# Performance work log

Measured on AMD Instinct MI355X. Metric: run time of the kernel, lower is better.

Reference implementation:

```python
import jax, jax.numpy as jnp
import numpy as np

EPS = 1e-8      # GumbelTopK background epsilon
TAU = 0.01      # relaxation temperature
NEG = -1e9      # mask-out value for already-selected patches
PATCH = (64, 64, 64)


def patchify(x, ps):
    """[B,C,H,W,D] -> [B*Hn*Wn*Dn, C, Hp, Wp, Dp] (non-overlapping tiles)."""
    B, C, H, W, D = x.shape
    hp, wp, dp = ps
    hn, wn, dn = H // hp, W // wp, D // dp
    x = x.reshape(B, C, hn, hp, wn, wp, dn, dp)
    x = x.transpose(0, 2, 4, 6, 1, 3, 5, 7)  # B,Hn,Wn,Dn,C,Hp,Wp,Dp
    return x.reshape(B * hn * wn * dn, C, hp, wp, dp)


def gumbel_topk(logit_flat, gumbel, k, tau):
    """Iterative Gumbel top-k: hard one-hots (stop-grad) + relaxed soft-hots."""
    perturbed = logit_flat + gumbel  # [B, N]

    def step(mask, _):
        s = jax.nn.softmax((perturbed + mask) / tau, axis=-1)  # [B, N]
        hard = jax.nn.one_hot(jnp.argmax(s, axis=-1), s.shape[-1], dtype=s.dtype)
        return mask + hard * NEG, (jax.lax.stop_gradient(hard), s)

    _, (one_hots, soft_hots) = jax.lax.scan(
        step, jnp.zeros_like(perturbed), None, length=k)
    return one_hots, soft_hots  # each [K, B, N]


def reference(image, label, logit, background_mask, gumbel, k):
    B = logit.shape[0]
    img_patches = patchify(image, PATCH)  # [N, C, 64,64,64]
    lab_patches = patchify(label, PATCH)  # [N, 1, 64,64,64]

    log_mask = jnp.log(jnp.maximum(1.0 - background_mask, EPS))
    masked_logit = logit + log_mask                       # [B,1,Hn,Wn,Dn]
    flat = masked_logit.reshape(B, -1)                    # [B, N]

    one_h, soft_h = gumbel_topk(flat, gumbel, k, TAU)     # [K,B,N]
    K = one_h.shape[0]
    one_f = one_h.reshape(K, -1)                          # [K, B*N]
    soft_f = soft_h.reshape(K, -1)

    # TRAIN mode: image weighted by one_hot*soft_hot, label (LAB) by one_hot only
    img_out = jnp.einsum('nchwd,kn->kchwd', img_patches, one_f * soft_f)
    lab_out = jnp.einsum('nchwd,kn->kchwd', lab_patches, one_f)
    return img_out, lab_out, masked_logit


def setup_inputs():
    key = jax.random.key(0)
    k1, k2, k3, k4, k5 = jax.random.split(key, 5)
    image = jax.random.normal(k1, (1, 4, 256, 256, 256), jnp.float32)
    label = jax.random.uniform(k2, (1, 1, 256, 256, 256), jnp.float32)
    logit = jax.random.normal(k3, (1, 1, 4, 4, 4), jnp.float32)
    background_mask = jax.random.uniform(k4, (1, 1, 4, 4, 4), jnp.float32)
    u = jax.random.uniform(k5, (1, 64), jnp.float32, 1e-6, 1.0 - 1e-6)
    gumbel = -jnp.log(-jnp.log(u))
    return {"image": image, "label": label, "logit": logit,
            "background_mask": background_mask, "gumbel": gumbel, "k": 8}
```

## Files before the change

### kernel.cpp

```cpp
#include <hip/hip_runtime.h>

#define TAU_INV 100.0f
#define EPSB    1e-8f
#define NEGV    -1e9f

typedef float v4f __attribute__((ext_vector_type(4)));

__global__ void stk_select(const float* __restrict__ logit,
                           const float* __restrict__ bg,
                           const float* __restrict__ gumbel,
                           float* __restrict__ ml_out,
                           int*   __restrict__ sel_idx,
                           float* __restrict__ sel_w,
                           int K) {
    int t = threadIdx.x;

    float lm = logf(fmaxf(1.0f - bg[t], EPSB));
    float ml = logit[t] + lm;
    ml_out[t] = ml;
    float pv = ml + gumbel[t];
    float mk = 0.0f;

    for (int k = 0; k < K; ++k) {
        float v   = pv + mk;
        float bv  = v;
        int   bi  = t;
        #pragma unroll
        for (int off = 32; off >= 1; off >>= 1) {
            float vo = __shfl_xor(bv, off);
            int   io = __shfl_xor(bi, off);
            if (vo > bv || (vo == bv && io < bi)) { bv = vo; bi = io; }
        }
        float e = __expf((v - bv) * TAU_INV);
        #pragma unroll
        for (int off = 32; off >= 1; off >>= 1)
            e += __shfl_xor(e, off);

        if (t == 0) {
            sel_idx[k] = bi;
            sel_w[k]   = 1.0f / e;
        }
        if (t == bi) mk += NEGV;
    }
}

__global__ void stk_gather(const v4f* __restrict__ img,
                           const v4f* __restrict__ lab,
                           v4f* __restrict__ out,
                           const int*   __restrict__ sel_idx,
                           const float* __restrict__ sel_w,
                           int nImg4, int nTot4) {
    int tid = blockIdx.x * blockDim.x + threadIdx.x;
    if (tid >= nTot4) return;

    if (tid < nImg4) {
        int v   = tid;
        int dp4 = v & 15;
        int wp  = (v >> 4)  & 63;
        int hp  = (v >> 10) & 63;
        int c   = (v >> 16) & 3;
        int k   = v >> 18;
        int n   = sel_idx[k];
        int hn  = n >> 4, wn = (n >> 2) & 3, dn = n & 3;
        int src = c * 4194304 + (hn * 64 + hp) * 16384 + (wn * 64 + wp) * 64 + dn * 16 + dp4;
        v4f d = __builtin_nontemporal_load(&img[src]);
        float w = sel_w[k];
        d *= w;
        __builtin_nontemporal_store(d, &out[tid]);
    } else {
        int u   = tid - nImg4;
        int dp4 = u & 15;
        int wp  = (u >> 4)  & 63;
        int hp  = (u >> 10) & 63;
        int k   = u >> 16;
        int n   = sel_idx[k];
        int hn  = n >> 4, wn = (n >> 2) & 3, dn = n & 3;
        int src = (hn * 64 + hp) * 16384 + (wn * 64 + wp) * 64 + dn * 16 + dp4;
        v4f d = __builtin_nontemporal_load(&lab[src]);
        __builtin_nontemporal_store(d, &out[tid]);
    }
}

extern "C" void kernel_launch(void* const* d_in, const int* in_sizes, int n_in,
                              void* d_out, int out_size, void* d_ws, size_t ws_size,
                              hipStream_t stream) {
    const float* image  = (const float*)d_in[0];
    const float* label  = (const float*)d_in[1];
    const float* logit  = (const float*)d_in[2];
    const float* bg     = (const float*)d_in[3];
    const float* gumbel = (const float*)d_in[4];
    int K = (out_size - 64) / (5 * 64 * 64 * 64);

    float* out     = (float*)d_out;
    int*   sel_idx = (int*)d_ws;
    float* sel_w   = (float*)((char*)d_ws + 64);
    float* ml_out  = out + (size_t)K * 1310720;

    stk_select<<<1, 64, 0, stream>>>(logit, bg, gumbel, ml_out, sel_idx, sel_w, K);

    int nImg4 = K * 4 * 65536;
    int nTot4 = nImg4 + K * 65536;
    int blocks = (nTot4 + 255) / 256;
    stk_gather<<<blocks, 256, 0, stream>>>((const v4f*)image, (const v4f*)label,
                                           (v4f*)out, sel_idx, sel_w, nImg4, nTot4);
}
```

Measured before the change: 352.4 us.

## Fuse top-k selection into gather kernel with per-block redundant selection

Merges the single-block selection kernel and the gather kernel into one launch. Every block recomputes the Gumbel top-k selection in its first wavefront and keeps the indices and weights in shared memory, so the second kernel launch and the global workspace round-trip go away. The gather becomes a grid-stride loop with four elements per thread, which cuts the block count by four. The cost is redundant selection work in every block, a serial K-step shuffle chain paid before each block's loads can start, and fewer blocks in flight.

```diff
diff --git a/kernel.cpp b/kernel.cpp
--- a/kernel.cpp
+++ b/kernel.cpp
@@ -6,78 +6,75 @@
 
 typedef float v4f __attribute__((ext_vector_type(4)));
 
-__global__ void stk_select(const float* __restrict__ logit,
-                           const float* __restrict__ bg,
-                           const float* __restrict__ gumbel,
-                           float* __restrict__ ml_out,
-                           int*   __restrict__ sel_idx,
-                           float* __restrict__ sel_w,
-                           int K) {
-    int t = threadIdx.x;
+__global__ __launch_bounds__(256) void stk_fused(
+    const float* __restrict__ logit,
+    const float* __restrict__ bg,
+    const float* __restrict__ gumbel,
+    const v4f*   __restrict__ img,
+    const v4f*   __restrict__ lab,
+    v4f*         __restrict__ out,
+    float*       __restrict__ ml_out,
+    int K, int nImg4, int nTot4)
+{
+    __shared__ int   s_idx[32];
+    __shared__ float s_w[32];
+    const int t = threadIdx.x;
 
-    float lm = logf(fmaxf(1.0f - bg[t], EPSB));
-    float ml = logit[t] + lm;
-    ml_out[t] = ml;
-    float pv = ml + gumbel[t];
-    float mk = 0.0f;
+    if (t < 64) {
+        float lm = logf(fmaxf(1.0f - bg[t], EPSB));
+        float ml = logit[t] + lm;
+        if (blockIdx.x == 0) ml_out[t] = ml;
+        float pv = ml + gumbel[t];
+        float mk = 0.0f;
 
-    for (int k = 0; k < K; ++k) {
-        float v   = pv + mk;
-        float bv  = v;
-        int   bi  = t;
-        #pragma unroll
-        for (int off = 32; off >= 1; off >>= 1) {
-            float vo = __shfl_xor(bv, off);
-            int   io = __shfl_xor(bi, off);
-            if (vo > bv || (vo == bv && io < bi)) { bv = vo; bi = io; }
+        for (int k = 0; k < K; ++k) {
+            float v  = pv + mk;
+            float bv = v;
+            int   bi = t;
+            #pragma unroll
+            for (int off = 32; off >= 1; off >>= 1) {
+                float vo = __shfl_xor(bv, off);
+                int   io = __shfl_xor(bi, off);
+                if (vo > bv || (vo == bv && io < bi)) { bv = vo; bi = io; }
+            }
+            float e = __expf((v - bv) * TAU_INV);
+            #pragma unroll
+            for (int off = 32; off >= 1; off >>= 1)
+                e += __shfl_xor(e, off);
+
+            if (t == 0) { s_idx[k] = bi; s_w[k] = 1.0f / e; }
+            if (t == bi) mk += NEGV;
         }
-        float e = __expf((v - bv) * TAU_INV);
-        #pragma unroll
-        for (int off = 32; off >= 1; off >>= 1)
-            e += __shfl_xor(e, off);
+    }
+    __syncthreads();
 
-        if (t == 0) {
-            sel_idx[k] = bi;
-            sel_w[k]   = 1.0f / e;
+    const int stride = gridDim.x * blockDim.x;
+    for (int tid = blockIdx.x * blockDim.x + t; tid < nTot4; tid += stride) {
+        if (tid < nImg4) {
+            int v   = tid;
+            int dp4 = v & 15;
+            int wp  = (v >> 4)  & 63;
+            int hp  = (v >> 10) & 63;
+            int c   = (v >> 16) & 3;
+            int k   = v >> 18;
+            int n   = s_idx[k];
+            int hn  = n >> 4, wn = (n >> 2) & 3, dn = n & 3;
+            int src = c * 4194304 + (hn * 64 + hp) * 16384 + (wn * 64 + wp) * 64 + dn * 16 + dp4;
+            v4f d = __builtin_nontemporal_load(&img[src]);
+            d *= s_w[k];
+            __builtin_nontemporal_store(d, &out[tid]);
+        } else {
+            int u   = tid - nImg4;
+            int dp4 = u & 15;
+            int wp  = (u >> 4)  & 63;
+            int hp  = (u >> 10) & 63;
+            int k   = u >> 16;
+            int n   = s_idx[k];
+            int hn  = n >> 4, wn = (n >> 2) & 3, dn = n & 3;
+            int src = (hn * 64 + hp) * 16384 + (wn * 64 + wp) * 64 + dn * 16 + dp4;
+            v4f d = __builtin_nontemporal_load(&lab[src]);
+            __builtin_nontemporal_store(d, &out[tid]);
         }
-        if (t == bi) mk += NEGV;
-    }
-}
-
-__global__ void stk_gather(const v4f* __restrict__ img,
-                           const v4f* __restrict__ lab,
-                           v4f* __restrict__ out,
-                           const int*   __restrict__ sel_idx,
-                           const float* __restrict__ sel_w,
-                           int nImg4, int nTot4) {
-    int tid = blockIdx.x * blockDim.x + threadIdx.x;
-    if (tid >= nTot4) return;
-
-    if (tid < nImg4) {
-        int v   = tid;
-        int dp4 = v & 15;
-        int wp  = (v >> 4)  & 63;
-        int hp  = (v >> 10) & 63;
-        int c   = (v >> 16) & 3;
-        int k   = v >> 18;
-        int n   = sel_idx[k];
-        int hn  = n >> 4, wn = (n >> 2) & 3, dn = n & 3;
-        int src = c * 4194304 + (hn * 64 + hp) * 16384 + (wn * 64 + wp) * 64 + dn * 16 + dp4;
-        v4f d = __builtin_nontemporal_load(&img[src]);
-        float w = sel_w[k];
-        d *= w;
-        __builtin_nontemporal_store(d, &out[tid]);
-    } else {
-        int u   = tid - nImg4;
-        int dp4 = u & 15;
-        int wp  = (u >> 4)  & 63;
-        int hp  = (u >> 10) & 63;
-        int k   = u >> 16;
-        int n   = sel_idx[k];
-        int hn  = n >> 4, wn = (n >> 2) & 3, dn = n & 3;
-        int src = (hn * 64 + hp) * 16384 + (wn * 64 + wp) * 64 + dn * 16 + dp4;
-        v4f d = __builtin_nontemporal_load(&lab[src]);
-        __builtin_nontemporal_store(d, &out[tid]);
     }
 }
 
@@ -91,16 +88,15 @@
     const float* gumbel = (const float*)d_in[4];
     int K = (out_size - 64) / (5 * 64 * 64 * 64);
 
-    float* out     = (float*)d_out;
-    int*   sel_idx = (int*)d_ws;
-    float* sel_w   = (float*)((char*)d_ws + 64);
-    float* ml_out  = out + (size_t)K * 1310720;
-
-    stk_select<<<1, 64, 0, stream>>>(logit, bg, gumbel, ml_out, sel_idx, sel_w, K);
+    float* out    = (float*)d_out;
+    float* ml_out = out + (size_t)K * 1310720;
 
     int nImg4 = K * 4 * 65536;
     int nTot4 = nImg4 + K * 65536;
-    int blocks = (nTot4 + 255) / 256;
-    stk_gather<<<blocks, 256, 0, stream>>>((const v4f*)image, (const v4f*)label,
-                                           (v4f*)out, sel_idx, sel_w, nImg4, nTot4);
+
+    int blocks = (nTot4 + 1023) / 1024;
+    if (blocks < 1) blocks = 1;
+    stk_fused<<<blocks, 256, 0, stream>>>(logit, bg, gumbel,
+                                          (const v4f*)image, (const v4f*)label,
+                                          (v4f*)out, ml_out, K, nImg4, nTot4);
 }
```

Measured after the change: 360.1 us. 1.02x slower.
